# Kernel optimization log

Measured on AMD Instinct MI355X. Metric: run time of the kernel, lower is better.

Reference implementation:

```python
import jax, jax.numpy as jnp
import numpy as np
import math

B, T, C, H = 8, 1024, 768, 12
HD = C // H  # 64


def setup_inputs() -> dict:
    key = jax.random.key(0)
    k1, k2, k3 = jax.random.split(key, 3)
    x = jax.random.normal(k1, (B, T, C), dtype=jnp.float32)
    W_attn = jax.random.normal(k2, (C, 3 * C), dtype=jnp.float32) * 0.02
    b_attn = jnp.zeros((3 * C,), dtype=jnp.float32)
    W_proj = jax.random.normal(k3, (C, C), dtype=jnp.float32) * (0.02 / math.sqrt(2 * 12))
    b_proj = jnp.zeros((C,), dtype=jnp.float32)
    return {"x": x, "W_attn": W_attn, "b_attn": b_attn, "W_proj": W_proj, "b_proj": b_proj}


def reference(x, W_attn, b_attn, W_proj, b_proj):
    Bx, Tx, Cx = x.shape
    qkv = x @ W_attn + b_attn                        # [B,T,3C]
    # faithful to original: reshape to (B,T,H,3*HD) then split last axis
    qkv = qkv.reshape(Bx, Tx, H, 3 * HD).transpose(0, 2, 1, 3)  # [B,H,T,3*HD]
    q, k, v = jnp.split(qkv, 3, axis=-1)             # each [B,H,T,HD]
    att = jnp.einsum('bhqd,bhkd->bhqk', q, k) / math.sqrt(HD)
    causal = jnp.tril(jnp.ones((Tx, Tx), dtype=bool))
    att = jnp.where(causal, att, -jnp.inf)
    att = jax.nn.softmax(att, axis=-1)
    y = jnp.einsum('bhqk,bhkd->bhqd', att, v)        # [B,H,T,HD]
    y = y.transpose(0, 2, 1, 3).reshape(Bx, Tx, Cx)  # [B,T,C]
    return y @ W_proj + b_proj
```

## Files before the change

kernel.cpp:

```cpp
#include <hip/hip_runtime.h>
#include <hip/hip_bf16.h>


#define TDIM 1024
#define CDIM 768
#define NDIM 2304

typedef __attribute__((ext_vector_type(8))) short bf16x8;
typedef __attribute__((ext_vector_type(8))) unsigned short u16x8;
typedef __attribute__((ext_vector_type(4))) float f32x4;

__device__ __forceinline__ unsigned short f2bf(float f) {
    unsigned int u;
    __builtin_memcpy(&u, &f, 4);
    u += 0x7FFFu + ((u >> 16) & 1u);
    return (unsigned short)(u >> 16);
}

__device__ __forceinline__ void async_copy16(void* lds, const void* g) {
    __builtin_amdgcn_global_load_lds(
        (const __attribute__((address_space(1))) void*)g,
        (__attribute__((address_space(3))) void*)lds, 16, 0, 0);
}

__global__ __launch_bounds__(256) void cast_x(const float* __restrict__ x,
                                              unsigned short* __restrict__ xb) {
    const size_t i = ((size_t)blockIdx.x * 256 + threadIdx.x) * 4;
    float4 v = *(const float4*)&x[i];
    ushort4 s;
    s.x = f2bf(v.x); s.y = f2bf(v.y); s.z = f2bf(v.z); s.w = f2bf(v.w);
    *(ushort4*)&xb[i] = s;
}

template <int N>
__global__ __launch_bounds__(256) void transpose_cast(const float* __restrict__ W,
                                                      unsigned short* __restrict__ Wt) {
    __shared__ float tile[32][33];
    const int n0 = blockIdx.x * 32;
    const int k0 = blockIdx.y * 32;
    const int tx = threadIdx.x & 31;
    const int ty = threadIdx.x >> 5;
#pragma unroll
    for (int i = 0; i < 4; ++i)
        tile[ty + i * 8][tx] = W[(size_t)(k0 + ty + i * 8) * N + n0 + tx];
    __syncthreads();
#pragma unroll
    for (int i = 0; i < 4; ++i)
        Wt[(size_t)(n0 + ty + i * 8) * CDIM + k0 + tx] = f2bf(tile[tx][ty + i * 8]);
}

__global__ __launch_bounds__(256) void qkv_mfma(
    const unsigned short* __restrict__ xb, const unsigned short* __restrict__ Wt,
    const float* __restrict__ bias,
    unsigned short* __restrict__ Q, unsigned short* __restrict__ Kd,
    unsigned short* __restrict__ V)
{
    const int n0 = blockIdx.x * 128;
    const int m0 = blockIdx.y * 128;
    const int tid = threadIdx.x;
    const int lane = tid & 63;
    const int w = tid >> 6;
    const int wm = w & 1;
    const int wn = w >> 1;
    const int lm = lane & 15;
    const int lq = lane >> 4;

    __shared__ __align__(16) unsigned short As[128 * 32];
    __shared__ __align__(16) unsigned short Bs[128 * 32];

    f32x4 acc[4][4] = {};

    const int srow = lane >> 2;
    const int schunk = lane & 3;

    for (int k0 = 0; k0 < CDIM; k0 += 32) {
        __syncthreads();
#pragma unroll
        for (int c = 0; c < 2; ++c) {
            const int rbase = c * 64 + w * 16;
            async_copy16(&As[rbase * 32],
                         &xb[(size_t)(m0 + rbase + srow) * CDIM + k0 + schunk * 8]);
            async_copy16(&Bs[rbase * 32],
                         &Wt[(size_t)(n0 + rbase + srow) * CDIM + k0 + schunk * 8]);
        }
        __syncthreads();

        bf16x8 a[4], b[4];
#pragma unroll
        for (int mi = 0; mi < 4; ++mi)
            a[mi] = *(const bf16x8*)&As[(wm * 64 + mi * 16 + lm) * 32 + lq * 8];
#pragma unroll
        for (int ni = 0; ni < 4; ++ni)
            b[ni] = *(const bf16x8*)&Bs[(wn * 64 + ni * 16 + lm) * 32 + lq * 8];
#pragma unroll
        for (int mi = 0; mi < 4; ++mi)
#pragma unroll
            for (int ni = 0; ni < 4; ++ni)
                acc[mi][ni] = __builtin_amdgcn_mfma_f32_16x16x32_bf16(
                    a[mi], b[ni], acc[mi][ni], 0, 0, 0);
    }

#pragma unroll
    for (int ni = 0; ni < 4; ++ni) {
        const int gn = n0 + wn * 64 + ni * 16 + lm;
        const float bb = bias[gn];
        const int h = gn / 192;
        const int rr = gn % 192;
        const int which = rr >> 6;
        const int d = rr & 63;
        unsigned short* dst = (which == 0) ? Q : ((which == 1) ? Kd : V);
#pragma unroll
        for (int mi = 0; mi < 4; ++mi) {
#pragma unroll
            for (int r = 0; r < 4; ++r) {
                const int gm = m0 + wm * 64 + mi * 16 + lq * 4 + r;
                const int bidx = gm >> 10;
                const int t = gm & 1023;
                dst[(((size_t)bidx * 12 + h) * TDIM + t) * 64 + d] = f2bf(acc[mi][ni][r] + bb);
            }
        }
    }
}

__global__ __launch_bounds__(256) void attn_mfma(
    const unsigned short* __restrict__ Q, const unsigned short* __restrict__ K,
    const unsigned short* __restrict__ V, unsigned short* __restrict__ Y)
{
    const int qt = blockIdx.x;
    const int bh = blockIdx.y;
    const int q0 = qt * 128;
    const int tid = threadIdx.x;
    const int lane = tid & 63;
    const int w = tid >> 6;
    const int lm = lane & 15;
    const int lq = lane >> 4;

    __shared__ __align__(16) unsigned short Ks[64][72];
    __shared__ __align__(16) unsigned short Vts[64][72];
    __shared__ __align__(16) unsigned short Ps[4][32][72];

    const unsigned short* Qb = Q + (size_t)bh * TDIM * 64;
    const unsigned short* Kb = K + (size_t)bh * TDIM * 64;
    const unsigned short* Vb = V + (size_t)bh * TDIM * 64;
    unsigned short* Yb = Y + (size_t)bh * TDIM * 64;

    unsigned short* PsFlat = &Ps[0][0][0];
#pragma unroll
    for (int it = 0; it < 4; ++it) {
        const int idx = tid + it * 256;
        const int r = idx >> 3;
        const int c = idx & 7;
        *(u16x8*)&PsFlat[r * 72 + c * 8] =
            *(const u16x8*)&Qb[(size_t)(q0 + r) * 64 + c * 8];
    }
    __syncthreads();

    bf16x8 aq[2][2];
#pragma unroll
    for (int mt = 0; mt < 2; ++mt)
#pragma unroll
        for (int kc = 0; kc < 2; ++kc)
            aq[mt][kc] = *(const bf16x8*)&PsFlat[(w * 32 + mt * 16 + lm) * 72 + kc * 32 + lq * 8];

    float l_p[2][4] = {};
    f32x4 o[2][4] = {};

    const int nkt = 2 * qt + 2;
    const float SC = 0.125f * 1.44269504f;

    for (int kt = 0; kt < nkt; ++kt) {
        const int kbase = kt * 64;
        __syncthreads();
#pragma unroll
        for (int it = 0; it < 2; ++it) {
            const int idx = tid + it * 256;
            const int r = idx >> 3;
            const int c = idx & 7;
            *(u16x8*)&Ks[r][c * 8] =
                *(const u16x8*)&Kb[(size_t)(kbase + r) * 64 + c * 8];
        }
        {
            const int key = tid >> 2;
            const int dq = tid & 3;
#pragma unroll
            for (int it = 0; it < 4; ++it) {
                const int d0 = dq * 4 + it * 16;
                ushort4 v = *(const ushort4*)&Vb[(size_t)(kbase + key) * 64 + d0];
                Vts[d0 + 0][key] = v.x;
                Vts[d0 + 1][key] = v.y;
                Vts[d0 + 2][key] = v.z;
                Vts[d0 + 3][key] = v.w;
            }
        }
        __syncthreads();

        const bool diag = (kt >= 2 * qt);

#pragma unroll
        for (int mt = 0; mt < 2; ++mt) {
            float pf[4][4];
#pragma unroll
            for (int nt = 0; nt < 4; ++nt) {
                f32x4 s = {};
#pragma unroll
                for (int kc = 0; kc < 2; ++kc) {
                    bf16x8 b = *(const bf16x8*)&Ks[nt * 16 + lm][kc * 32 + lq * 8];
                    s = __builtin_amdgcn_mfma_f32_16x16x32_bf16(aq[mt][kc], b, s, 0, 0, 0);
                }
                const int keyg = kbase + nt * 16 + lm;
#pragma unroll
                for (int r = 0; r < 4; ++r) {
                    float p = __builtin_amdgcn_exp2f(s[r] * SC);
                    if (diag) {
                        const int qg = q0 + w * 32 + mt * 16 + lq * 4 + r;
                        if (keyg > qg) p = 0.f;
                    }
                    pf[nt][r] = p;
                }
            }
#pragma unroll
            for (int r = 0; r < 4; ++r) {
                l_p[mt][r] += pf[0][r] + pf[1][r] + pf[2][r] + pf[3][r];
#pragma unroll
                for (int nt = 0; nt < 4; ++nt)
                    Ps[w][mt * 16 + lq * 4 + r][nt * 16 + lm] = f2bf(pf[nt][r]);
            }
        }

#pragma unroll
        for (int mt = 0; mt < 2; ++mt) {
            bf16x8 ap[2];
#pragma unroll
            for (int kc = 0; kc < 2; ++kc)
                ap[kc] = *(const bf16x8*)&Ps[w][mt * 16 + lm][kc * 32 + lq * 8];
#pragma unroll
            for (int nt = 0; nt < 4; ++nt) {
#pragma unroll
                for (int kc = 0; kc < 2; ++kc) {
                    bf16x8 bv = *(const bf16x8*)&Vts[nt * 16 + lm][kc * 32 + lq * 8];
                    o[mt][nt] = __builtin_amdgcn_mfma_f32_16x16x32_bf16(ap[kc], bv, o[mt][nt], 0, 0, 0);
                }
            }
        }
    }

#pragma unroll
    for (int mt = 0; mt < 2; ++mt)
#pragma unroll
        for (int r = 0; r < 4; ++r) {
            float l = l_p[mt][r];
#pragma unroll
            for (int off = 1; off < 16; off <<= 1) l += __shfl_xor(l, off);
            const float inv = 1.0f / l;
            const int qg = q0 + w * 32 + mt * 16 + lq * 4 + r;
#pragma unroll
            for (int nt = 0; nt < 4; ++nt)
                Yb[(size_t)qg * 64 + nt * 16 + lm] = f2bf(o[mt][nt][r] * inv);
        }
}

__global__ __launch_bounds__(256) void proj_mfma(
    const unsigned short* __restrict__ Y, const unsigned short* __restrict__ Wt,
    const float* __restrict__ bias, float* __restrict__ out)
{
    const int n0 = blockIdx.x * 128;
    const int m0 = blockIdx.y * 128;
    const int tid = threadIdx.x;
    const int lane = tid & 63;
    const int w = tid >> 6;
    const int wm = w & 1;
    const int wn = w >> 1;
    const int lm = lane & 15;
    const int lq = lane >> 4;

    __shared__ __align__(16) unsigned short As[128 * 32];
    __shared__ __align__(16) unsigned short Bs[128 * 32];

    f32x4 acc[4][4] = {};

    const int srow = lane >> 2;
    const int schunk = lane & 3;

    for (int k0 = 0; k0 < CDIM; k0 += 32) {
        const int h = k0 >> 6;
        const int inner = k0 & 63;
        __syncthreads();
#pragma unroll
        for (int c = 0; c < 2; ++c) {
            const int rbase = c * 64 + w * 16;
            const int m = m0 + rbase + srow;
            const int bidx = m >> 10;
            const int t = m & 1023;
            async_copy16(&As[rbase * 32],
                         &Y[(((size_t)bidx * 12 + h) * TDIM + t) * 64 + inner + schunk * 8]);
            async_copy16(&Bs[rbase * 32],
                         &Wt[(size_t)(n0 + rbase + srow) * CDIM + k0 + schunk * 8]);
        }
        __syncthreads();

        bf16x8 a[4], b[4];
#pragma unroll
        for (int mi = 0; mi < 4; ++mi)
            a[mi] = *(const bf16x8*)&As[(wm * 64 + mi * 16 + lm) * 32 + lq * 8];
#pragma unroll
        for (int ni = 0; ni < 4; ++ni)
            b[ni] = *(const bf16x8*)&Bs[(wn * 64 + ni * 16 + lm) * 32 + lq * 8];
#pragma unroll
        for (int mi = 0; mi < 4; ++mi)
#pragma unroll
            for (int ni = 0; ni < 4; ++ni)
                acc[mi][ni] = __builtin_amdgcn_mfma_f32_16x16x32_bf16(
                    a[mi], b[ni], acc[mi][ni], 0, 0, 0);
    }

#pragma unroll
    for (int ni = 0; ni < 4; ++ni) {
        const int gn = n0 + wn * 64 + ni * 16 + lm;
        const float bb = bias[gn];
#pragma unroll
        for (int mi = 0; mi < 4; ++mi) {
#pragma unroll
            for (int r = 0; r < 4; ++r) {
                const int gm = m0 + wm * 64 + mi * 16 + lq * 4 + r;
                out[(size_t)gm * CDIM + gn] = acc[mi][ni][r] + bb;
            }
        }
    }
}

extern "C" void kernel_launch(void* const* d_in, const int* in_sizes, int n_in,
                              void* d_out, int out_size, void* d_ws, size_t ws_size,
                              hipStream_t stream) {
    const float* x      = (const float*)d_in[0];
    const float* W_attn = (const float*)d_in[1];
    const float* b_attn = (const float*)d_in[2];
    const float* W_proj = (const float*)d_in[3];
    const float* b_proj = (const float*)d_in[4];
    float* out = (float*)d_out;

    const size_t per = (size_t)8 * 12 * 1024 * 64;
    unsigned short* Q   = (unsigned short*)d_ws;
    unsigned short* K   = Q + per;
    unsigned short* V   = K + per;
    unsigned short* xb  = V + per;
    unsigned short* Wta = xb + (size_t)8192 * CDIM;
    unsigned short* Wtp = Wta + (size_t)NDIM * CDIM;

    cast_x<<<dim3(6144), 256, 0, stream>>>(x, xb);
    transpose_cast<NDIM><<<dim3(72, 24), 256, 0, stream>>>(W_attn, Wta);
    transpose_cast<CDIM><<<dim3(24, 24), 256, 0, stream>>>(W_proj, Wtp);

    qkv_mfma<<<dim3(18, 64), 256, 0, stream>>>(xb, Wta, b_attn, Q, K, V);
    attn_mfma<<<dim3(8, 96), 256, 0, stream>>>(Q, K, V, Q);
    proj_mfma<<<dim3(6, 64), 256, 0, stream>>>(Q, Wtp, b_proj, out);
}
```

Before: 221.0 us.

## Pair causal query tiles per block and emit V pre-transposed from QKV GEMM

The attention kernel now processes two query tiles per block (tile i and 7-i), so every block does the same amount of causal work and each K/V tile loaded into LDS is shared by both query tiles. The grid drops from 8x96 to 4x96 blocks. The QKV GEMM writes V in a [d][t] transposed layout with 4-wide stores, which replaces the scalar LDS transpose scatter inside the attention loop with plain vector copies. Q fragments are loaded straight from global memory instead of being staged through LDS. The cost is double the accumulator registers per thread, which may lower occupancy, and fewer blocks to fill the GPU.

```diff
diff --git a/kernel.cpp b/kernel.cpp
--- a/kernel.cpp
+++ b/kernel.cpp
@@ -53,7 +53,7 @@
     const unsigned short* __restrict__ xb, const unsigned short* __restrict__ Wt,
     const float* __restrict__ bias,
     unsigned short* __restrict__ Q, unsigned short* __restrict__ Kd,
-    unsigned short* __restrict__ V)
+    unsigned short* __restrict__ Vt)
 {
     const int n0 = blockIdx.x * 128;
     const int m0 = blockIdx.y * 128;
@@ -108,27 +108,108 @@
         const int rr = gn % 192;
         const int which = rr >> 6;
         const int d = rr & 63;
-        unsigned short* dst = (which == 0) ? Q : ((which == 1) ? Kd : V);
-#pragma unroll
-        for (int mi = 0; mi < 4; ++mi) {
-#pragma unroll
-            for (int r = 0; r < 4; ++r) {
-                const int gm = m0 + wm * 64 + mi * 16 + lq * 4 + r;
-                const int bidx = gm >> 10;
-                const int t = gm & 1023;
-                dst[(((size_t)bidx * 12 + h) * TDIM + t) * 64 + d] = f2bf(acc[mi][ni][r] + bb);
+        if (which == 2) {
+#pragma unroll
+            for (int mi = 0; mi < 4; ++mi) {
+                const int gm0 = m0 + wm * 64 + mi * 16 + lq * 4;
+                const int bidx = gm0 >> 10;
+                const int t0 = gm0 & 1023;
+                ushort4 sv;
+                sv.x = f2bf(acc[mi][ni][0] + bb);
+                sv.y = f2bf(acc[mi][ni][1] + bb);
+                sv.z = f2bf(acc[mi][ni][2] + bb);
+                sv.w = f2bf(acc[mi][ni][3] + bb);
+                *(ushort4*)&Vt[(((size_t)bidx * 12 + h) * 64 + d) * TDIM + t0] = sv;
             }
-        }
-    }
-}
+        } else {
+            unsigned short* dst = (which == 0) ? Q : Kd;
+#pragma unroll
+            for (int mi = 0; mi < 4; ++mi) {
+#pragma unroll
+                for (int r = 0; r < 4; ++r) {
+                    const int gm = m0 + wm * 64 + mi * 16 + lq * 4 + r;
+                    const int bidx = gm >> 10;
+                    const int t = gm & 1023;
+                    dst[(((size_t)bidx * 12 + h) * TDIM + t) * 64 + d] = f2bf(acc[mi][ni][r] + bb);
+                }
+            }
+        }
+    }
+}
+
+#define ATTN_TILE(aq, q0t, l_p, o, diagflag) do {                               \
+    const bool diag_ = (diagflag);                                              \
+    _Pragma("unroll")                                                           \
+    for (int mt = 0; mt < 2; ++mt) {                                            \
+        float pf[4][4];                                                         \
+        _Pragma("unroll")                                                       \
+        for (int nt = 0; nt < 4; ++nt) {                                        \
+            f32x4 s = {};                                                       \
+            _Pragma("unroll")                                                   \
+            for (int kc = 0; kc < 2; ++kc) {                                    \
+                bf16x8 bfrag = *(const bf16x8*)&Ks[nt * 16 + lm][kc * 32 + lq * 8]; \
+                s = __builtin_amdgcn_mfma_f32_16x16x32_bf16(aq[mt][kc], bfrag, s, 0, 0, 0); \
+            }                                                                   \
+            const int keyg = kbase + nt * 16 + lm;                              \
+            _Pragma("unroll")                                                   \
+            for (int r = 0; r < 4; ++r) {                                       \
+                float p = __builtin_amdgcn_exp2f(s[r] * SC);                    \
+                if (diag_) {                                                    \
+                    const int qg = (q0t) + w * 32 + mt * 16 + lq * 4 + r;       \
+                    if (keyg > qg) p = 0.f;                                     \
+                }                                                               \
+                pf[nt][r] = p;                                                  \
+            }                                                                   \
+        }                                                                       \
+        _Pragma("unroll")                                                       \
+        for (int r = 0; r < 4; ++r) {                                           \
+            l_p[mt][r] += pf[0][r] + pf[1][r] + pf[2][r] + pf[3][r];            \
+            _Pragma("unroll")                                                   \
+            for (int nt = 0; nt < 4; ++nt)                                      \
+                Ps[w][mt * 16 + lq * 4 + r][nt * 16 + lm] = f2bf(pf[nt][r]);    \
+        }                                                                       \
+    }                                                                           \
+    _Pragma("unroll")                                                           \
+    for (int mt = 0; mt < 2; ++mt) {                                            \
+        bf16x8 ap[2];                                                           \
+        _Pragma("unroll")                                                       \
+        for (int kc = 0; kc < 2; ++kc)                                          \
+            ap[kc] = *(const bf16x8*)&Ps[w][mt * 16 + lm][kc * 32 + lq * 8];    \
+        _Pragma("unroll")                                                       \
+        for (int nt = 0; nt < 4; ++nt) {                                        \
+            _Pragma("unroll")                                                   \
+            for (int kc = 0; kc < 2; ++kc) {                                    \
+                bf16x8 bv = *(const bf16x8*)&Vts[nt * 16 + lm][kc * 32 + lq * 8]; \
+                o[mt][nt] = __builtin_amdgcn_mfma_f32_16x16x32_bf16(ap[kc], bv, o[mt][nt], 0, 0, 0); \
+            }                                                                   \
+        }                                                                       \
+    }                                                                           \
+} while (0)
+
+#define ATTN_EPI(q0t, l_p, o) do {                                              \
+    _Pragma("unroll")                                                           \
+    for (int mt = 0; mt < 2; ++mt)                                              \
+        _Pragma("unroll")                                                       \
+        for (int r = 0; r < 4; ++r) {                                           \
+            float l = l_p[mt][r];                                               \
+            _Pragma("unroll")                                                   \
+            for (int off = 1; off < 16; off <<= 1) l += __shfl_xor(l, off);     \
+            const float inv = 1.0f / l;                                         \
+            const int qg = (q0t) + w * 32 + mt * 16 + lq * 4 + r;               \
+            _Pragma("unroll")                                                   \
+            for (int nt = 0; nt < 4; ++nt)                                      \
+                Yb[(size_t)qg * 64 + nt * 16 + lm] = f2bf(o[mt][nt][r] * inv);  \
+        }                                                                       \
+} while (0)
 
 __global__ __launch_bounds__(256) void attn_mfma(
     const unsigned short* __restrict__ Q, const unsigned short* __restrict__ K,
-    const unsigned short* __restrict__ V, unsigned short* __restrict__ Y)
+    const unsigned short* __restrict__ Vt, unsigned short* __restrict__ Y)
 {
-    const int qt = blockIdx.x;
+    const int pi = blockIdx.x;
     const int bh = blockIdx.y;
-    const int q0 = qt * 128;
+    const int qtA = pi, qtB = 7 - pi;
+    const int q0A = qtA * 128, q0B = qtB * 128;
     const int tid = threadIdx.x;
     const int lane = tid & 63;
     const int w = tid >> 6;
@@ -141,34 +222,26 @@
 
     const unsigned short* Qb = Q + (size_t)bh * TDIM * 64;
     const unsigned short* Kb = K + (size_t)bh * TDIM * 64;
-    const unsigned short* Vb = V + (size_t)bh * TDIM * 64;
+    const unsigned short* Vtb = Vt + (size_t)bh * 64 * TDIM;
     unsigned short* Yb = Y + (size_t)bh * TDIM * 64;
 
-    unsigned short* PsFlat = &Ps[0][0][0];
-#pragma unroll
-    for (int it = 0; it < 4; ++it) {
-        const int idx = tid + it * 256;
-        const int r = idx >> 3;
-        const int c = idx & 7;
-        *(u16x8*)&PsFlat[r * 72 + c * 8] =
-            *(const u16x8*)&Qb[(size_t)(q0 + r) * 64 + c * 8];
-    }
-    __syncthreads();
-
-    bf16x8 aq[2][2];
+    bf16x8 aqA[2][2], aqB[2][2];
 #pragma unroll
     for (int mt = 0; mt < 2; ++mt)
 #pragma unroll
-        for (int kc = 0; kc < 2; ++kc)
-            aq[mt][kc] = *(const bf16x8*)&PsFlat[(w * 32 + mt * 16 + lm) * 72 + kc * 32 + lq * 8];
-
-    float l_p[2][4] = {};
-    f32x4 o[2][4] = {};
-
-    const int nkt = 2 * qt + 2;
+        for (int kc = 0; kc < 2; ++kc) {
+            aqA[mt][kc] = *(const bf16x8*)&Qb[(size_t)(q0A + w * 32 + mt * 16 + lm) * 64 + kc * 32 + lq * 8];
+            aqB[mt][kc] = *(const bf16x8*)&Qb[(size_t)(q0B + w * 32 + mt * 16 + lm) * 64 + kc * 32 + lq * 8];
+        }
+
+    float lA[2][4] = {}, lB[2][4] = {};
+    f32x4 oA[2][4] = {}, oB[2][4] = {};
+
     const float SC = 0.125f * 1.44269504f;
-
-    for (int kt = 0; kt < nkt; ++kt) {
+    const int nktA = 2 * qtA + 2;
+    const int nktB = 2 * qtB + 2;
+
+    for (int kt = 0; kt < nktB; ++kt) {
         const int kbase = kt * 64;
         __syncthreads();
 #pragma unroll
@@ -178,85 +251,17 @@
             const int c = idx & 7;
             *(u16x8*)&Ks[r][c * 8] =
                 *(const u16x8*)&Kb[(size_t)(kbase + r) * 64 + c * 8];
-        }
-        {
-            const int key = tid >> 2;
-            const int dq = tid & 3;
-#pragma unroll
-            for (int it = 0; it < 4; ++it) {
-                const int d0 = dq * 4 + it * 16;
-                ushort4 v = *(const ushort4*)&Vb[(size_t)(kbase + key) * 64 + d0];
-                Vts[d0 + 0][key] = v.x;
-                Vts[d0 + 1][key] = v.y;
-                Vts[d0 + 2][key] = v.z;
-                Vts[d0 + 3][key] = v.w;
-            }
-        }
-        __syncthreads();
-
-        const bool diag = (kt >= 2 * qt);
-
-#pragma unroll
-        for (int mt = 0; mt < 2; ++mt) {
-            float pf[4][4];
-#pragma unroll
-            for (int nt = 0; nt < 4; ++nt) {
-                f32x4 s = {};
-#pragma unroll
-                for (int kc = 0; kc < 2; ++kc) {
-                    bf16x8 b = *(const bf16x8*)&Ks[nt * 16 + lm][kc * 32 + lq * 8];
-                    s = __builtin_amdgcn_mfma_f32_16x16x32_bf16(aq[mt][kc], b, s, 0, 0, 0);
-                }
-                const int keyg = kbase + nt * 16 + lm;
-#pragma unroll
-                for (int r = 0; r < 4; ++r) {
-                    float p = __builtin_amdgcn_exp2f(s[r] * SC);
-                    if (diag) {
-                        const int qg = q0 + w * 32 + mt * 16 + lq * 4 + r;
-                        if (keyg > qg) p = 0.f;
-                    }
-                    pf[nt][r] = p;
-                }
-            }
-#pragma unroll
-            for (int r = 0; r < 4; ++r) {
-                l_p[mt][r] += pf[0][r] + pf[1][r] + pf[2][r] + pf[3][r];
-#pragma unroll
-                for (int nt = 0; nt < 4; ++nt)
-                    Ps[w][mt * 16 + lq * 4 + r][nt * 16 + lm] = f2bf(pf[nt][r]);
-            }
-        }
-
-#pragma unroll
-        for (int mt = 0; mt < 2; ++mt) {
-            bf16x8 ap[2];
-#pragma unroll
-            for (int kc = 0; kc < 2; ++kc)
-                ap[kc] = *(const bf16x8*)&Ps[w][mt * 16 + lm][kc * 32 + lq * 8];
-#pragma unroll
-            for (int nt = 0; nt < 4; ++nt) {
-#pragma unroll
-                for (int kc = 0; kc < 2; ++kc) {
-                    bf16x8 bv = *(const bf16x8*)&Vts[nt * 16 + lm][kc * 32 + lq * 8];
-                    o[mt][nt] = __builtin_amdgcn_mfma_f32_16x16x32_bf16(ap[kc], bv, o[mt][nt], 0, 0, 0);
-                }
-            }
-        }
-    }
-
-#pragma unroll
-    for (int mt = 0; mt < 2; ++mt)
-#pragma unroll
-        for (int r = 0; r < 4; ++r) {
-            float l = l_p[mt][r];
-#pragma unroll
-            for (int off = 1; off < 16; off <<= 1) l += __shfl_xor(l, off);
-            const float inv = 1.0f / l;
-            const int qg = q0 + w * 32 + mt * 16 + lq * 4 + r;
-#pragma unroll
-            for (int nt = 0; nt < 4; ++nt)
-                Yb[(size_t)qg * 64 + nt * 16 + lm] = f2bf(o[mt][nt][r] * inv);
-        }
+            *(u16x8*)&Vts[r][c * 8] =
+                *(const u16x8*)&Vtb[(size_t)r * TDIM + kbase + c * 8];
+        }
+        __syncthreads();
+
+        ATTN_TILE(aqB, q0B, lB, oB, (kt >= 2 * qtB));
+        if (kt < nktA) ATTN_TILE(aqA, q0A, lA, oA, (kt >= 2 * qtA));
+    }
+
+    ATTN_EPI(q0A, lA, oA);
+    ATTN_EPI(q0B, lB, oB);
 }
 
 __global__ __launch_bounds__(256) void proj_mfma(
@@ -341,8 +346,8 @@
     const size_t per = (size_t)8 * 12 * 1024 * 64;
     unsigned short* Q   = (unsigned short*)d_ws;
     unsigned short* K   = Q + per;
-    unsigned short* V   = K + per;
-    unsigned short* xb  = V + per;
+    unsigned short* Vt  = K + per;
+    unsigned short* xb  = Vt + per;
     unsigned short* Wta = xb + (size_t)8192 * CDIM;
     unsigned short* Wtp = Wta + (size_t)NDIM * CDIM;
 
@@ -350,7 +355,7 @@
     transpose_cast<NDIM><<<dim3(72, 24), 256, 0, stream>>>(W_attn, Wta);
     transpose_cast<CDIM><<<dim3(24, 24), 256, 0, stream>>>(W_proj, Wtp);
 
-    qkv_mfma<<<dim3(18, 64), 256, 0, stream>>>(xb, Wta, b_attn, Q, K, V);
-    attn_mfma<<<dim3(8, 96), 256, 0, stream>>>(Q, K, V, Q);
+    qkv_mfma<<<dim3(18, 64), 256, 0, stream>>>(xb, Wta, b_attn, Q, K, Vt);
+    attn_mfma<<<dim3(4, 96), 256, 0, stream>>>(Q, K, Vt, Q);
     proj_mfma<<<dim3(6, 64), 256, 0, stream>>>(Q, Wtp, b_proj, out);
 }
```

Result: slower. 242.0 us (+9.5%).
